# Optimization experiments

Measured on AMD Instinct MI355X. Metric: run time of the kernel, lower is better.

The kernel has to match this reference:

```python
import jax, jax.numpy as jnp
import numpy as np

N, D, U, E, B = 8192, 1024, 512, 8, 8


def setup_inputs() -> dict:
    key = jax.random.key(0)
    ks = jax.random.split(key, 8)
    x = jax.random.normal(ks[0], (N, D), dtype=jnp.float32)
    # stacked per-expert parameters (Dense + KolmogorovLayer)
    W1 = jax.random.normal(ks[1], (E, D, U), dtype=jnp.float32) * 0.02
    b1 = jnp.zeros((E, U), dtype=jnp.float32)
    proj = jax.random.normal(ks[2], (E, U, U), dtype=jnp.float32) * 0.02
    ctrl = jax.random.normal(ks[3], (E, B, U), dtype=jnp.float32) * 0.1
    scaling = jnp.ones((E, U), dtype=jnp.float32)
    # gating Dense
    Wg = jax.random.normal(ks[4], (D, E), dtype=jnp.float32) * 0.02
    bg = jnp.zeros((E,), dtype=jnp.float32)
    return {"x": x, "W1": W1, "b1": b1, "proj": proj, "ctrl": ctrl,
            "scaling": scaling, "Wg": Wg, "bg": bg}


def reference(x, W1, b1, proj, ctrl, scaling, Wg, bg):
    num_bases = ctrl.shape[1]
    # expert Dense + swish: [E, N, U]
    h = jax.nn.swish(jnp.einsum('nd,edu->enu', x, W1) + b1[:, None, :])
    # KolmogorovLayer: projection -> sigmoid -> gaussian-RBF B-spline basis
    z = jnp.einsum('enu,euv->env', h, proj)
    xn = jax.nn.sigmoid(z)                                   # [E, N, U] in (0,1)
    knots = jnp.linspace(0.0, 1.0, num_bases)                # [B]
    dist = (xn[..., None] - knots) ** 2                      # [E, N, U, B]
    basis = jnp.exp(-dist / (2.0 * (1.0 / num_bases) ** 2))
    basis = basis / (jnp.sum(basis, axis=-1, keepdims=True) + 1e-6)
    # contract bases with control points per unit, then scale: [E, N, U]
    expert_out = jnp.einsum('enub,ebu->enu', basis, ctrl) * scaling[:, None, :]
    # gating (inference path): hard one-hot argmax of logits
    logits = x @ Wg + bg                                     # [N, E]
    gate = jax.nn.one_hot(jnp.argmax(logits, axis=-1), logits.shape[-1],
                          dtype=x.dtype)                     # [N, E]
    # weighted sum over experts -> [N, U]
    return jnp.einsum('enu,ne->nu', expert_out, gate)
```

## Files before the change

### kernel.cpp

```cpp
#include <hip/hip_runtime.h>
#include <hip/hip_bf16.h>
#include <stdint.h>

#define NTOK 8192
#define DDIM 1024
#define UDIM 512
#define NEXP 8
#define MT_MAX 136

typedef __attribute__((ext_vector_type(8))) short bf16x8;
typedef __attribute__((ext_vector_type(4))) float f32x4;


__device__ __forceinline__ unsigned short f2bf(float f) {
  unsigned int u = __float_as_uint(f);
  u += 0x7FFFu + ((u >> 16) & 1u);
  return (unsigned short)(u >> 16);
}

__device__ __forceinline__ void gload16(const void* g, void* lds) {
  __builtin_amdgcn_global_load_lds(
      (__attribute__((address_space(1))) void*)(uintptr_t)g,
      (__attribute__((address_space(3))) void*)(uint32_t)(uintptr_t)lds,
      16, 0, 0);
}


__global__ __launch_bounds__(256) void k_prep(const float* __restrict__ x,
                                              const float* __restrict__ Wg,
                                              const float* __restrict__ bg,
                                              int* __restrict__ eidx) {
  __shared__ float WgT[8][1040];
  const int t = threadIdx.x;
#pragma unroll
  for (int r = 0; r < 32; ++r)
    WgT[t & 7][r * 32 + (t >> 3)] = Wg[r * 256 + t];
  __syncthreads();

  const int lane = t & 63;
  const int n = (blockIdx.x << 2) + (t >> 6);
  const float* xr = x + (size_t)n * DDIM;
  float acc[8] = {0.f, 0.f, 0.f, 0.f, 0.f, 0.f, 0.f, 0.f};
#pragma unroll
  for (int c = 0; c < 4; ++c) {
    const float4 xv = *(const float4*)(xr + c * 256 + lane * 4);
#pragma unroll
    for (int e = 0; e < 8; ++e) {
      const float4 wv = *(const float4*)(&WgT[e][c * 256 + lane * 4]);
      acc[e] = fmaf(xv.x, wv.x, acc[e]);
      acc[e] = fmaf(xv.y, wv.y, acc[e]);
      acc[e] = fmaf(xv.z, wv.z, acc[e]);
      acc[e] = fmaf(xv.w, wv.w, acc[e]);
    }
  }
#pragma unroll
  for (int e = 0; e < 8; ++e) {
#pragma unroll
    for (int o = 32; o > 0; o >>= 1) acc[e] += __shfl_xor(acc[e], o, 64);
  }
  if (lane == 0) {
    int best = 0;
    float bv = acc[0] + bg[0];
#pragma unroll
    for (int e2 = 1; e2 < 8; ++e2) {
      const float v = acc[e2] + bg[e2];
      if (v > bv) { bv = v; best = e2; }
    }
    eidx[n] = best;
  }
}


__global__ void k_pack(const float* __restrict__ W1, const float* __restrict__ proj,
                       unsigned short* __restrict__ W1p, unsigned short* __restrict__ projp) {
  __shared__ float tile[64][65];
  const int z = blockIdx.z;
  const int R = (z < 8) ? DDIM : UDIM;
  const int r0 = blockIdx.y << 6;
  if (r0 >= R) return;
  const int c0 = blockIdx.x << 6;
  const float* src = (z < 8) ? (W1 + (size_t)z * DDIM * UDIM)
                             : (proj + (size_t)(z - 8) * UDIM * UDIM);
  unsigned short* dst = (z < 8) ? (W1p + (size_t)z * DDIM * UDIM)
                                : (projp + (size_t)(z - 8) * UDIM * UDIM);
  const int t = threadIdx.x;
#pragma unroll
  for (int i = 0; i < 4; ++i) {
    const int ri = (t >> 4) + i * 16;
    const int ci = (t & 15) * 4;
    const float4 v = *(const float4*)(src + (size_t)(r0 + ri) * UDIM + c0 + ci);
    tile[ri][ci] = v.x; tile[ri][ci + 1] = v.y; tile[ri][ci + 2] = v.z; tile[ri][ci + 3] = v.w;
  }
  __syncthreads();
  const int cc = t >> 2, ch = t & 3;
#pragma unroll
  for (int j = 0; j < 2; ++j) {
    const int kt = (r0 >> 5) + j;
    union { bf16x8 v; unsigned short u[8]; } pk;
#pragma unroll
    for (int q = 0; q < 8; ++q) pk.u[q] = f2bf(tile[j * 32 + ch * 8 + q][cc]);
    *(bf16x8*)(dst + ((size_t)kt * UDIM + c0 + cc) * 32 + ch * 8) = pk.v;
  }
}


__global__ __launch_bounds__(1024) void k_sort(const int* __restrict__ eidx,
                                               int* __restrict__ perm_p,
                                               int* __restrict__ tile_expert,
                                               int* __restrict__ tile_rowlim) {
  __shared__ int hist[8][1024];
  __shared__ int tbase[9];
  const int t = threadIdx.x;

  int my[8], c[8] = {0, 0, 0, 0, 0, 0, 0, 0};
#pragma unroll
  for (int i = 0; i < 8; ++i) {
    my[i] = eidx[t * 8 + i];
#pragma unroll
    for (int b = 0; b < 8; ++b) c[b] += (my[i] == b);
  }
#pragma unroll
  for (int b = 0; b < 8; ++b) hist[b][t] = c[b];
  __syncthreads();

  for (int off = 1; off < 1024; off <<= 1) {
    int v[8];
#pragma unroll
    for (int b = 0; b < 8; ++b) v[b] = (t >= off) ? hist[b][t - off] : 0;
    __syncthreads();
#pragma unroll
    for (int b = 0; b < 8; ++b) hist[b][t] += v[b];
    __syncthreads();
  }

  if (t == 0) {
    int run = 0;
    for (int e = 0; e < 8; ++e) { tbase[e] = run; run += (hist[e][1023] + 63) >> 6; }
    tbase[8] = run;
  }
  __syncthreads();

  int base[8];
#pragma unroll
  for (int b = 0; b < 8; ++b) base[b] = (tbase[b] << 6) + hist[b][t] - c[b];
#pragma unroll
  for (int b = 0; b < 8; ++b) {
    int p = base[b];
#pragma unroll
    for (int i = 0; i < 8; ++i)
      if (my[i] == b) perm_p[p++] = t * 8 + i;
  }

  if (t < MT_MAX) {
    int e = -1, rl = 0;
#pragma unroll
    for (int q = 0; q < 8; ++q) {
      if (t >= tbase[q] && t < tbase[q + 1]) {
        e = q;
        const int r = hist[q][1023] - (t - tbase[q]) * 64;
        rl = r < 64 ? r : 64;
      }
    }
    tile_expert[t] = e;
    tile_rowlim[t] = rl;
  }
}


__global__ __launch_bounds__(256) void k_gemm1(
    const float* __restrict__ x, const unsigned short* __restrict__ W1p,
    const float* __restrict__ b1, const int* __restrict__ perm_p,
    const int* __restrict__ tile_expert, const int* __restrict__ tile_rowlim,
    unsigned short* __restrict__ Hp) {
  __shared__ __align__(16) short Ab[2][64 * 32];
  __shared__ __align__(16) short Bb[2][128 * 32];
  __shared__ int rows_s[64];

  const int Mt = blockIdx.x;
  const int e = tile_expert[Mt];
  if (e < 0) return;
  const int Nt = blockIdx.y;
  const int rowlim = tile_rowlim[Mt];

  const int t = threadIdx.x;
  const int w = t >> 6, wr = w >> 1, wc = w & 1;
  const int lane = t & 63, ln15 = lane & 15, g = lane >> 4;

  if (t < 64) rows_s[t] = perm_p[Mt * 64 + (t < rowlim ? t : 0)];
  __syncthreads();

  const int arow = t >> 2;
  const int ah = (t & 3) ^ ((arow >> 1) & 3);
  const float* xrow = x + (size_t)rows_s[arow] * DDIM + ah * 8;
  const unsigned short* Bpan = W1p + ((size_t)e * 32 * UDIM + Nt * 128) * 32;

  float4 av0, av1;
  auto issueA = [&](int kt) {
    const float* s = xrow + kt * 32;
    av0 = *(const float4*)s; av1 = *(const float4*)(s + 4);
  };
  auto writeA = [&](int buf) {
    union { bf16x8 v; unsigned short u[8]; } pk;
    pk.u[0] = f2bf(av0.x); pk.u[1] = f2bf(av0.y); pk.u[2] = f2bf(av0.z); pk.u[3] = f2bf(av0.w);
    pk.u[4] = f2bf(av1.x); pk.u[5] = f2bf(av1.y); pk.u[6] = f2bf(av1.z); pk.u[7] = f2bf(av1.w);
    *(bf16x8*)((char*)Ab[buf] + t * 16) = pk.v;
  };
  auto issueB = [&](int kt, int buf) {
#pragma unroll
    for (int j = 0; j < 2; ++j) {
      const int c = t + j * 256;
      const int u2 = c >> 2, h = (c & 3) ^ ((u2 >> 1) & 3);
      gload16(Bpan + (size_t)kt * UDIM * 32 + u2 * 32 + h * 8,
              (char*)Bb[buf] + (c & ~63) * 16);
    }
  };

  f32x4 acc[2][4];
  const f32x4 z4 = {0.f, 0.f, 0.f, 0.f};
#pragma unroll
  for (int a = 0; a < 2; ++a)
#pragma unroll
    for (int b = 0; b < 4; ++b) acc[a][b] = z4;

  issueA(0); issueB(0, 0); writeA(0);
  __syncthreads();
  int cur = 0;
  for (int kt = 0; kt < 32; ++kt) {
    const int nb = cur ^ 1;
    if (kt < 31) { issueA(kt + 1); issueB(kt + 1, nb); }
    bf16x8 af[2], bf_[4];
#pragma unroll
    for (int mt = 0; mt < 2; ++mt) {
      const int r = wr * 32 + mt * 16 + ln15;
      af[mt] = *(const bf16x8*)((const char*)Ab[cur] + r * 64 + (g ^ ((r >> 1) & 3)) * 16);
    }
#pragma unroll
    for (int nt = 0; nt < 4; ++nt) {
      const int c2 = wc * 64 + nt * 16 + ln15;
      bf_[nt] = *(const bf16x8*)((const char*)Bb[cur] + c2 * 64 + (g ^ ((c2 >> 1) & 3)) * 16);
    }
#pragma unroll
    for (int mt = 0; mt < 2; ++mt)
#pragma unroll
      for (int nt = 0; nt < 4; ++nt)
        acc[mt][nt] = __builtin_amdgcn_mfma_f32_16x16x32_bf16(af[mt], bf_[nt], acc[mt][nt], 0, 0, 0);
    if (kt < 31) writeA(nb);
    __syncthreads();
    cur = nb;
  }

  float bv[4];
#pragma unroll
  for (int nt = 0; nt < 4; ++nt)
    bv[nt] = b1[e * UDIM + Nt * 128 + wc * 64 + nt * 16 + ln15];
#pragma unroll
  for (int mt = 0; mt < 2; ++mt) {
#pragma unroll
    for (int nt = 0; nt < 4; ++nt) {
      const int colg = Nt * 128 + wc * 64 + nt * 16 + ln15;
      unsigned short* hp = Hp + ((size_t)(Mt * 16 + (colg >> 5)) * 64) * 32 + (colg & 31);
#pragma unroll
      for (int r = 0; r < 4; ++r) {
        const int row = wr * 32 + mt * 16 + g * 4 + r;
        const float a = acc[mt][nt][r] + bv[nt];
        hp[(size_t)row * 32] = f2bf(a * __builtin_amdgcn_rcpf(1.f + __expf(-a)));
      }
    }
  }
}


__global__ __launch_bounds__(256) void k_gemm2(
    const unsigned short* __restrict__ Hp, const unsigned short* __restrict__ projp,
    const float* __restrict__ ctrl, const float* __restrict__ scaling,
    const int* __restrict__ perm_p, const int* __restrict__ tile_expert,
    const int* __restrict__ tile_rowlim, float* __restrict__ out) {
  __shared__ __align__(16) short Ab[2][64 * 32];
  __shared__ __align__(16) short Bb[2][64 * 32];
  __shared__ int tok_s[64];

  const int Mt = blockIdx.x;
  const int e = tile_expert[Mt];
  if (e < 0) return;
  const int Nt = blockIdx.y;
  const int rowlim = tile_rowlim[Mt];

  const int t = threadIdx.x;
  const int w = t >> 6, wr = w >> 1, wc = w & 1;
  const int lane = t & 63, ln15 = lane & 15, g = lane >> 4;

  if (t < 64) tok_s[t] = perm_p[Mt * 64 + (t < rowlim ? t : 0)];
  __syncthreads();

  const int srow = t >> 2;
  const int sh = (t & 3) ^ ((srow >> 1) & 3);
  const unsigned short* Apan = Hp + ((size_t)Mt * 16 * 64) * 32;
  const unsigned short* Bpan = projp + ((size_t)e * 16 * UDIM + Nt * 64) * 32;

  auto stage = [&](int kt, int buf) {
    gload16(Apan + (size_t)kt * 64 * 32 + srow * 32 + sh * 8,
            (char*)Ab[buf] + (t & ~63) * 16);
    gload16(Bpan + (size_t)kt * UDIM * 32 + srow * 32 + sh * 8,
            (char*)Bb[buf] + (t & ~63) * 16);
  };

  f32x4 acc[2][2];
  const f32x4 z4 = {0.f, 0.f, 0.f, 0.f};
  acc[0][0] = z4; acc[0][1] = z4; acc[1][0] = z4; acc[1][1] = z4;

  stage(0, 0);
  __syncthreads();
  int cur = 0;
  for (int kt = 0; kt < 16; ++kt) {
    const int nb = cur ^ 1;
    if (kt < 15) stage(kt + 1, nb);
    bf16x8 af[2], bf_[2];
#pragma unroll
    for (int mt = 0; mt < 2; ++mt) {
      const int r = wr * 32 + mt * 16 + ln15;
      af[mt] = *(const bf16x8*)((const char*)Ab[cur] + r * 64 + (g ^ ((r >> 1) & 3)) * 16);
    }
#pragma unroll
    for (int nt = 0; nt < 2; ++nt) {
      const int c2 = wc * 32 + nt * 16 + ln15;
      bf_[nt] = *(const bf16x8*)((const char*)Bb[cur] + c2 * 64 + (g ^ ((c2 >> 1) & 3)) * 16);
    }
#pragma unroll
    for (int mt = 0; mt < 2; ++mt)
#pragma unroll
      for (int nt = 0; nt < 2; ++nt)
        acc[mt][nt] = __builtin_amdgcn_mfma_f32_16x16x32_bf16(af[mt], bf_[nt], acc[mt][nt], 0, 0, 0);
    __syncthreads();
    cur = nb;
  }

  const float M = 0.27086949f;
  float cv[2][8], sc[2];
#pragma unroll
  for (int nt = 0; nt < 2; ++nt) {
    const int colg = Nt * 64 + wc * 32 + nt * 16 + ln15;
    sc[nt] = scaling[e * UDIM + colg];
#pragma unroll
    for (int b = 0; b < 8; ++b) cv[nt][b] = ctrl[((size_t)e * 8 + b) * UDIM + colg];
  }
#pragma unroll
  for (int mt = 0; mt < 2; ++mt) {
#pragma unroll
    for (int r = 0; r < 4; ++r) {
      const int row = wr * 32 + mt * 16 + g * 4 + r;
      if (row < rowlim) {
        const int tok = tok_s[row];
#pragma unroll
        for (int nt = 0; nt < 2; ++nt) {
          const int colg = Nt * 64 + wc * 32 + nt * 16 + ln15;
          const float z = acc[mt][nt][r];
          const float xn = __builtin_amdgcn_rcpf(1.f + __expf(-z));
          float q = __expf(-32.f * xn * xn);
          float rr = __expf(xn * (64.f / 7.f) - (32.f / 49.f));
          float s = 0.f, dc = 0.f;
#pragma unroll
          for (int b = 0; b < 8; ++b) {
            s += q;
            dc = fmaf(q, cv[nt][b], dc);
            q *= rr;
            rr *= M;
          }
          out[(size_t)tok * UDIM + colg] = dc * __builtin_amdgcn_rcpf(s + 1e-6f) * sc[nt];
        }
      }
    }
  }
}


extern "C" void kernel_launch(void* const* d_in, const int* in_sizes, int n_in,
                              void* d_out, int out_size, void* d_ws, size_t ws_size,
                              hipStream_t stream) {
  const float* x       = (const float*)d_in[0];
  const float* W1      = (const float*)d_in[1];
  const float* b1      = (const float*)d_in[2];
  const float* proj    = (const float*)d_in[3];
  const float* ctrl    = (const float*)d_in[4];
  const float* scaling = (const float*)d_in[5];
  const float* Wg      = (const float*)d_in[6];
  const float* bg      = (const float*)d_in[7];
  float* out = (float*)d_out;
  char* ws = (char*)d_ws;

  int* eidx        = (int*)(ws + 0);
  int* perm_p      = (int*)(ws + 32768);
  int* tile_expert = (int*)(ws + 69632 + 64);
  int* tile_rowlim = (int*)(ws + 69632 + 640);
  unsigned short* W1p   = (unsigned short*)(ws + 131072);
  unsigned short* projp = (unsigned short*)(ws + 131072 + 8388608);
  unsigned short* Hp    = (unsigned short*)(ws + 131072 + 8388608 + 4194304);

  k_prep<<<NTOK / 4, 256, 0, stream>>>(x, Wg, bg, eidx);
  k_pack<<<dim3(UDIM / 64, DDIM / 64, 16), 256, 0, stream>>>(W1, proj, W1p, projp);
  k_sort<<<1, 1024, 0, stream>>>(eidx, perm_p, tile_expert, tile_rowlim);
  k_gemm1<<<dim3(MT_MAX, UDIM / 128), 256, 0, stream>>>(x, W1p, b1, perm_p,
                                                        tile_expert, tile_rowlim, Hp);
  k_gemm2<<<dim3(MT_MAX, UDIM / 64), 256, 0, stream>>>(Hp, projp, ctrl, scaling, perm_p,
                                                       tile_expert, tile_rowlim, out);
}
```

Before: 74.12 us.

## Fuse prep and pack kernels, pre-convert x to bf16, shrink gemm1 tiles, remap blocks

Merges the gating/argmax kernel and the weight packing kernel into one launch. The merged kernel also writes a bf16 copy of x, so gemm1 can stage A with async global-to-LDS loads instead of converting fp32 in registers. gemm1's N tile shrinks from 128 to 64, doubling block count. Both GEMMs use a 1D grid with a remap that spreads consecutive blocks across M tiles for better cache locality. The cost is an extra bf16 write and read of x, plus reading B panels twice as often.

```diff
diff --git a/kernel.cpp b/kernel.cpp
--- a/kernel.cpp
+++ b/kernel.cpp
@@ -26,80 +26,87 @@
 }
 
 
-__global__ __launch_bounds__(256) void k_prep(const float* __restrict__ x,
-                                              const float* __restrict__ Wg,
-                                              const float* __restrict__ bg,
-                                              int* __restrict__ eidx) {
-  __shared__ float WgT[8][1040];
+__global__ __launch_bounds__(256) void k_prep_pack(
+    const float* __restrict__ x, const float* __restrict__ Wg,
+    const float* __restrict__ bg, const float* __restrict__ W1,
+    const float* __restrict__ proj, unsigned short* __restrict__ xbf,
+    int* __restrict__ eidx, unsigned short* __restrict__ W1p,
+    unsigned short* __restrict__ projp) {
+  __shared__ __align__(16) char smem[8 * 1040 * 4];
   const int t = threadIdx.x;
-#pragma unroll
-  for (int r = 0; r < 32; ++r)
-    WgT[t & 7][r * 32 + (t >> 3)] = Wg[r * 256 + t];
-  __syncthreads();
-
-  const int lane = t & 63;
-  const int n = (blockIdx.x << 2) + (t >> 6);
-  const float* xr = x + (size_t)n * DDIM;
-  float acc[8] = {0.f, 0.f, 0.f, 0.f, 0.f, 0.f, 0.f, 0.f};
-#pragma unroll
-  for (int c = 0; c < 4; ++c) {
-    const float4 xv = *(const float4*)(xr + c * 256 + lane * 4);
+
+  if (blockIdx.x < 2048) {
+    float (*WgT)[1040] = (float(*)[1040])smem;
+#pragma unroll
+    for (int r = 0; r < 32; ++r)
+      WgT[t & 7][r * 32 + (t >> 3)] = Wg[r * 256 + t];
+    __syncthreads();
+
+    const int lane = t & 63;
+    const int n = (blockIdx.x << 2) + (t >> 6);
+    const float* xr = x + (size_t)n * DDIM;
+    unsigned short* xo = xbf + (size_t)n * DDIM;
+    float acc[8] = {0.f, 0.f, 0.f, 0.f, 0.f, 0.f, 0.f, 0.f};
+#pragma unroll
+    for (int c = 0; c < 4; ++c) {
+      const int d = c * 256 + lane * 4;
+      const float4 xv = *(const float4*)(xr + d);
+      ushort4 o;
+      o.x = f2bf(xv.x); o.y = f2bf(xv.y); o.z = f2bf(xv.z); o.w = f2bf(xv.w);
+      *(ushort4*)(xo + d) = o;
+#pragma unroll
+      for (int e = 0; e < 8; ++e) {
+        const float4 wv = *(const float4*)(&WgT[e][d]);
+        acc[e] = fmaf(xv.x, wv.x, acc[e]);
+        acc[e] = fmaf(xv.y, wv.y, acc[e]);
+        acc[e] = fmaf(xv.z, wv.z, acc[e]);
+        acc[e] = fmaf(xv.w, wv.w, acc[e]);
+      }
+    }
 #pragma unroll
     for (int e = 0; e < 8; ++e) {
-      const float4 wv = *(const float4*)(&WgT[e][c * 256 + lane * 4]);
-      acc[e] = fmaf(xv.x, wv.x, acc[e]);
-      acc[e] = fmaf(xv.y, wv.y, acc[e]);
-      acc[e] = fmaf(xv.z, wv.z, acc[e]);
-      acc[e] = fmaf(xv.w, wv.w, acc[e]);
-    }
-  }
-#pragma unroll
-  for (int e = 0; e < 8; ++e) {
-#pragma unroll
-    for (int o = 32; o > 0; o >>= 1) acc[e] += __shfl_xor(acc[e], o, 64);
-  }
-  if (lane == 0) {
-    int best = 0;
-    float bv = acc[0] + bg[0];
-#pragma unroll
-    for (int e2 = 1; e2 < 8; ++e2) {
-      const float v = acc[e2] + bg[e2];
-      if (v > bv) { bv = v; best = e2; }
-    }
-    eidx[n] = best;
-  }
-}
-
-
-__global__ void k_pack(const float* __restrict__ W1, const float* __restrict__ proj,
-                       unsigned short* __restrict__ W1p, unsigned short* __restrict__ projp) {
-  __shared__ float tile[64][65];
-  const int z = blockIdx.z;
-  const int R = (z < 8) ? DDIM : UDIM;
-  const int r0 = blockIdx.y << 6;
-  if (r0 >= R) return;
-  const int c0 = blockIdx.x << 6;
-  const float* src = (z < 8) ? (W1 + (size_t)z * DDIM * UDIM)
-                             : (proj + (size_t)(z - 8) * UDIM * UDIM);
-  unsigned short* dst = (z < 8) ? (W1p + (size_t)z * DDIM * UDIM)
-                                : (projp + (size_t)(z - 8) * UDIM * UDIM);
-  const int t = threadIdx.x;
-#pragma unroll
-  for (int i = 0; i < 4; ++i) {
-    const int ri = (t >> 4) + i * 16;
-    const int ci = (t & 15) * 4;
-    const float4 v = *(const float4*)(src + (size_t)(r0 + ri) * UDIM + c0 + ci);
-    tile[ri][ci] = v.x; tile[ri][ci + 1] = v.y; tile[ri][ci + 2] = v.z; tile[ri][ci + 3] = v.w;
-  }
-  __syncthreads();
-  const int cc = t >> 2, ch = t & 3;
-#pragma unroll
-  for (int j = 0; j < 2; ++j) {
-    const int kt = (r0 >> 5) + j;
-    union { bf16x8 v; unsigned short u[8]; } pk;
-#pragma unroll
-    for (int q = 0; q < 8; ++q) pk.u[q] = f2bf(tile[j * 32 + ch * 8 + q][cc]);
-    *(bf16x8*)(dst + ((size_t)kt * UDIM + c0 + cc) * 32 + ch * 8) = pk.v;
+#pragma unroll
+      for (int o = 32; o > 0; o >>= 1) acc[e] += __shfl_xor(acc[e], o, 64);
+    }
+    if (lane == 0) {
+      int best = 0;
+      float bv = acc[0] + bg[0];
+#pragma unroll
+      for (int e2 = 1; e2 < 8; ++e2) {
+        const float v = acc[e2] + bg[e2];
+        if (v > bv) { bv = v; best = e2; }
+      }
+      eidx[n] = best;
+    }
+  } else {
+    float (*tile)[65] = (float(*)[65])smem;
+    const int id = blockIdx.x - 2048;
+    const int c0 = (id & 7) << 6;
+    const int r0 = ((id >> 3) & 15) << 6;
+    const int z = id >> 7;
+    const int R = (z < 8) ? DDIM : UDIM;
+    if (r0 >= R) return;
+    const float* src = (z < 8) ? (W1 + (size_t)z * DDIM * UDIM)
+                               : (proj + (size_t)(z - 8) * UDIM * UDIM);
+    unsigned short* dst = (z < 8) ? (W1p + (size_t)z * DDIM * UDIM)
+                                  : (projp + (size_t)(z - 8) * UDIM * UDIM);
+#pragma unroll
+    for (int i = 0; i < 4; ++i) {
+      const int ri = (t >> 4) + i * 16;
+      const int ci = (t & 15) * 4;
+      const float4 v = *(const float4*)(src + (size_t)(r0 + ri) * UDIM + c0 + ci);
+      tile[ri][ci] = v.x; tile[ri][ci + 1] = v.y; tile[ri][ci + 2] = v.z; tile[ri][ci + 3] = v.w;
+    }
+    __syncthreads();
+    const int cc = t >> 2, ch = t & 3;
+#pragma unroll
+    for (int j = 0; j < 2; ++j) {
+      const int kt = (r0 >> 5) + j;
+      union { bf16x8 v; unsigned short u[8]; } pk;
+#pragma unroll
+      for (int q = 0; q < 8; ++q) pk.u[q] = f2bf(tile[j * 32 + ch * 8 + q][cc]);
+      *(bf16x8*)(dst + ((size_t)kt * UDIM + c0 + cc) * 32 + ch * 8) = pk.v;
+    }
   }
 }
 
@@ -168,18 +175,19 @@
 
 
 __global__ __launch_bounds__(256) void k_gemm1(
-    const float* __restrict__ x, const unsigned short* __restrict__ W1p,
+    const unsigned short* __restrict__ xbf, const unsigned short* __restrict__ W1p,
     const float* __restrict__ b1, const int* __restrict__ perm_p,
     const int* __restrict__ tile_expert, const int* __restrict__ tile_rowlim,
     unsigned short* __restrict__ Hp) {
   __shared__ __align__(16) short Ab[2][64 * 32];
-  __shared__ __align__(16) short Bb[2][128 * 32];
+  __shared__ __align__(16) short Bb[2][64 * 32];
   __shared__ int rows_s[64];
 
-  const int Mt = blockIdx.x;
+  const int orig = blockIdx.x;
+  const int wg = (orig & 7) * (MT_MAX * 8 / 8) + (orig >> 3);
+  const int Mt = wg >> 3, Nt = wg & 7;
   const int e = tile_expert[Mt];
   if (e < 0) return;
-  const int Nt = blockIdx.y;
   const int rowlim = tile_rowlim[Mt];
 
   const int t = threadIdx.x;
@@ -189,75 +197,56 @@
   if (t < 64) rows_s[t] = perm_p[Mt * 64 + (t < rowlim ? t : 0)];
   __syncthreads();
 
-  const int arow = t >> 2;
-  const int ah = (t & 3) ^ ((arow >> 1) & 3);
-  const float* xrow = x + (size_t)rows_s[arow] * DDIM + ah * 8;
-  const unsigned short* Bpan = W1p + ((size_t)e * 32 * UDIM + Nt * 128) * 32;
-
-  float4 av0, av1;
-  auto issueA = [&](int kt) {
-    const float* s = xrow + kt * 32;
-    av0 = *(const float4*)s; av1 = *(const float4*)(s + 4);
+  const int srow = t >> 2;
+  const int sh = (t & 3) ^ ((srow >> 1) & 3);
+  const unsigned short* arow = xbf + (size_t)rows_s[srow] * DDIM + sh * 8;
+  const unsigned short* Bpan = W1p + ((size_t)e * 32 * UDIM + Nt * 64) * 32;
+
+  auto stage = [&](int kt, int buf) {
+    gload16(arow + kt * 32, (char*)Ab[buf] + (t & ~63) * 16);
+    gload16(Bpan + (size_t)kt * UDIM * 32 + srow * 32 + sh * 8,
+            (char*)Bb[buf] + (t & ~63) * 16);
   };
-  auto writeA = [&](int buf) {
-    union { bf16x8 v; unsigned short u[8]; } pk;
-    pk.u[0] = f2bf(av0.x); pk.u[1] = f2bf(av0.y); pk.u[2] = f2bf(av0.z); pk.u[3] = f2bf(av0.w);
-    pk.u[4] = f2bf(av1.x); pk.u[5] = f2bf(av1.y); pk.u[6] = f2bf(av1.z); pk.u[7] = f2bf(av1.w);
-    *(bf16x8*)((char*)Ab[buf] + t * 16) = pk.v;
-  };
-  auto issueB = [&](int kt, int buf) {
-#pragma unroll
-    for (int j = 0; j < 2; ++j) {
-      const int c = t + j * 256;
-      const int u2 = c >> 2, h = (c & 3) ^ ((u2 >> 1) & 3);
-      gload16(Bpan + (size_t)kt * UDIM * 32 + u2 * 32 + h * 8,
-              (char*)Bb[buf] + (c & ~63) * 16);
-    }
-  };
-
-  f32x4 acc[2][4];
+
+  f32x4 acc[2][2];
   const f32x4 z4 = {0.f, 0.f, 0.f, 0.f};
-#pragma unroll
-  for (int a = 0; a < 2; ++a)
-#pragma unroll
-    for (int b = 0; b < 4; ++b) acc[a][b] = z4;
-
-  issueA(0); issueB(0, 0); writeA(0);
+  acc[0][0] = z4; acc[0][1] = z4; acc[1][0] = z4; acc[1][1] = z4;
+
+  stage(0, 0);
   __syncthreads();
   int cur = 0;
   for (int kt = 0; kt < 32; ++kt) {
     const int nb = cur ^ 1;
-    if (kt < 31) { issueA(kt + 1); issueB(kt + 1, nb); }
-    bf16x8 af[2], bf_[4];
+    if (kt < 31) stage(kt + 1, nb);
+    bf16x8 af[2], bf_[2];
 #pragma unroll
     for (int mt = 0; mt < 2; ++mt) {
       const int r = wr * 32 + mt * 16 + ln15;
       af[mt] = *(const bf16x8*)((const char*)Ab[cur] + r * 64 + (g ^ ((r >> 1) & 3)) * 16);
     }
 #pragma unroll
-    for (int nt = 0; nt < 4; ++nt) {
-      const int c2 = wc * 64 + nt * 16 + ln15;
+    for (int nt = 0; nt < 2; ++nt) {
+      const int c2 = wc * 32 + nt * 16 + ln15;
       bf_[nt] = *(const bf16x8*)((const char*)Bb[cur] + c2 * 64 + (g ^ ((c2 >> 1) & 3)) * 16);
     }
 #pragma unroll
     for (int mt = 0; mt < 2; ++mt)
 #pragma unroll
-      for (int nt = 0; nt < 4; ++nt)
+      for (int nt = 0; nt < 2; ++nt)
         acc[mt][nt] = __builtin_amdgcn_mfma_f32_16x16x32_bf16(af[mt], bf_[nt], acc[mt][nt], 0, 0, 0);
-    if (kt < 31) writeA(nb);
     __syncthreads();
     cur = nb;
   }
 
-  float bv[4];
-#pragma unroll
-  for (int nt = 0; nt < 4; ++nt)
-    bv[nt] = b1[e * UDIM + Nt * 128 + wc * 64 + nt * 16 + ln15];
+  float bv[2];
+#pragma unroll
+  for (int nt = 0; nt < 2; ++nt)
+    bv[nt] = b1[e * UDIM + Nt * 64 + wc * 32 + nt * 16 + ln15];
 #pragma unroll
   for (int mt = 0; mt < 2; ++mt) {
 #pragma unroll
-    for (int nt = 0; nt < 4; ++nt) {
-      const int colg = Nt * 128 + wc * 64 + nt * 16 + ln15;
+    for (int nt = 0; nt < 2; ++nt) {
+      const int colg = Nt * 64 + wc * 32 + nt * 16 + ln15;
       unsigned short* hp = Hp + ((size_t)(Mt * 16 + (colg >> 5)) * 64) * 32 + (colg & 31);
 #pragma unroll
       for (int r = 0; r < 4; ++r) {
@@ -279,10 +268,11 @@
   __shared__ __align__(16) short Bb[2][64 * 32];
   __shared__ int tok_s[64];
 
-  const int Mt = blockIdx.x;
+  const int orig = blockIdx.x;
+  const int wg = (orig & 7) * (MT_MAX * 8 / 8) + (orig >> 3);
+  const int Mt = wg >> 3, Nt = wg & 7;
   const int e = tile_expert[Mt];
   if (e < 0) return;
-  const int Nt = blockIdx.y;
   const int rowlim = tile_rowlim[Mt];
 
   const int t = threadIdx.x;
@@ -394,12 +384,12 @@
   unsigned short* W1p   = (unsigned short*)(ws + 131072);
   unsigned short* projp = (unsigned short*)(ws + 131072 + 8388608);
   unsigned short* Hp    = (unsigned short*)(ws + 131072 + 8388608 + 4194304);
-
-  k_prep<<<NTOK / 4, 256, 0, stream>>>(x, Wg, bg, eidx);
-  k_pack<<<dim3(UDIM / 64, DDIM / 64, 16), 256, 0, stream>>>(W1, proj, W1p, projp);
+  unsigned short* xbf   = (unsigned short*)(ws + 131072 + 8388608 + 4194304 + 9175040);
+
+  k_prep_pack<<<4096, 256, 0, stream>>>(x, Wg, bg, W1, proj, xbf, eidx, W1p, projp);
   k_sort<<<1, 1024, 0, stream>>>(eidx, perm_p, tile_expert, tile_rowlim);
-  k_gemm1<<<dim3(MT_MAX, UDIM / 128), 256, 0, stream>>>(x, W1p, b1, perm_p,
-                                                        tile_expert, tile_rowlim, Hp);
-  k_gemm2<<<dim3(MT_MAX, UDIM / 64), 256, 0, stream>>>(Hp, projp, ctrl, scaling, perm_p,
-                                                       tile_expert, tile_rowlim, out);
-}
+  k_gemm1<<<MT_MAX * 8, 256, 0, stream>>>(xbf, W1p, b1, perm_p,
+                                          tile_expert, tile_rowlim, Hp);
+  k_gemm2<<<MT_MAX * 8, 256, 0, stream>>>(Hp, projp, ctrl, scaling, perm_p,
+                                          tile_expert, tile_rowlim, out);
+}
```

New measurement: 66.83 us. 9.8% less time.
